# Performance work log

Measured on AMD Instinct MI355X. Metric: run time of the kernel, lower is better.

Reference implementation:

```python
import jax, jax.numpy as jnp
import numpy as np

B, E, T, MAX_LEN = 8192, 1024, 64, 20
EPS = 1e-08


def setup_inputs() -> dict:
    key = jax.random.key(0)
    ks = jax.random.split(key, 8)
    s = 1.0 / np.sqrt(E)
    return {
        "h_t": jax.random.normal(ks[0], (B, E), dtype=jnp.float32),
        "testing": 0,
        "emb": jax.random.normal(ks[1], (T, E), dtype=jnp.float32),
        "W_ih": jax.random.uniform(ks[2], (4 * E, E), minval=-s, maxval=s, dtype=jnp.float32),
        "W_hh": jax.random.uniform(ks[3], (4 * E, E), minval=-s, maxval=s, dtype=jnp.float32),
        "b_ih": jax.random.uniform(ks[4], (4 * E,), minval=-s, maxval=s, dtype=jnp.float32),
        "b_hh": jax.random.uniform(ks[5], (4 * E,), minval=-s, maxval=s, dtype=jnp.float32),
        "W1": jax.random.uniform(ks[6], (T, E), minval=-s, maxval=s, dtype=jnp.float32),
        "b1": jax.random.uniform(ks[7], (T,), minval=-s, maxval=s, dtype=jnp.float32),
    }


def reference(h_t, testing, emb, W_ih, W_hh, b_ih, b_hh, W1, b1):
    batch = h_t.shape[0]
    c0 = jnp.zeros_like(h_t)
    tok0 = jnp.zeros((batch,), dtype=jnp.int32)

    def step(carry, key_i):
        h, c, last = carry
        x = emb[last]  # [B, E] embedding lookup
        gates = x @ W_ih.T + b_ih + h @ W_hh.T + b_hh  # [B, 4E]
        i_g, f_g, g_g, o_g = jnp.split(gates, 4, axis=1)  # PyTorch LSTMCell gate order i,f,g,o
        i_g = jax.nn.sigmoid(i_g)
        f_g = jax.nn.sigmoid(f_g)
        g_g = jnp.tanh(g_g)
        o_g = jax.nn.sigmoid(o_g)
        c = f_g * c + i_g * g_g
        h = o_g * jnp.tanh(c)
        logits = h @ W1.T + b1  # [B, T]
        probs = jax.nn.softmax(logits, axis=1)
        greedy = jnp.argmax(probs, axis=1)
        if testing:
            a = greedy
            log_g = jnp.zeros((batch,), dtype=probs.dtype)
        else:
            a = jax.random.categorical(key_i, logits, axis=1)  # multinomial(probs, 1)
            log_g = jnp.log(jnp.take_along_axis(probs, a[:, None], axis=1))[:, 0]
        matches = (greedy == a).sum()
        p = probs + EPS
        ent = -(p * jnp.log(p)).sum()
        return (h, c, a), (log_g, a, ent, matches)

    keys = jax.random.split(jax.random.key(42), MAX_LEN)
    (_, _, _), (log_gs, toks, ents, matches) = jax.lax.scan(step, (h_t, c0, tok0), keys)
    utterance = toks.T  # [B, MAX_LEN]
    entropy = ents.sum()
    matches_argmax_count = matches.sum()
    stochastic_draws_count = batch * MAX_LEN
    return (log_gs, utterance, entropy, matches_argmax_count, stochastic_draws_count)
```

## Files before the change

### kernel.cpp

```cpp
#include <hip/hip_runtime.h>
#include <hip/hip_bf16.h>
#include <stdint.h>
#include <math.h>

#define BB   8192
#define EE   1024
#define GG   4096
#define TTK  64
#define LLEN 20

#define PRNG_PARTITIONABLE 1

typedef __attribute__((ext_vector_type(8)))  __bf16 bf16x8;
typedef __attribute__((ext_vector_type(4)))  __bf16 bf16x4;
typedef __attribute__((ext_vector_type(16))) float  f32x16;

__host__ __device__ __forceinline__ void tf2x32(unsigned k0, unsigned k1,
                                                unsigned x0, unsigned x1,
                                                unsigned& o0, unsigned& o1) {
  unsigned ks2 = k0 ^ k1 ^ 0x1BD11BDAu;
#define TFR(r) { x0 += x1; x1 = (x1 << (r)) | (x1 >> (32 - (r))); x1 ^= x0; }
  x0 += k0; x1 += k1;
  TFR(13) TFR(15) TFR(26) TFR(6)  x0 += k1;  x1 += ks2 + 1u;
  TFR(17) TFR(29) TFR(16) TFR(24) x0 += ks2; x1 += k0 + 2u;
  TFR(13) TFR(15) TFR(26) TFR(6)  x0 += k0;  x1 += k1 + 3u;
  TFR(17) TFR(29) TFR(16) TFR(24) x0 += k1;  x1 += ks2 + 4u;
  TFR(13) TFR(15) TFR(26) TFR(6)  x0 += ks2; x1 += k0 + 5u;
#undef TFR
  o0 = x0; o1 = x1;
}

__device__ __forceinline__ float wave_max64(float v) {
#pragma unroll
  for (int o = 32; o > 0; o >>= 1) v = fmaxf(v, __shfl_xor(v, o));
  return v;
}
__device__ __forceinline__ float wave_sum64(float v) {
#pragma unroll
  for (int o = 32; o > 0; o >>= 1) v += __shfl_xor(v, o);
  return v;
}
__device__ __forceinline__ void wave_argmax64(float v, int i, float& rv, int& ri) {
  rv = v; ri = i;
#pragma unroll
  for (int o = 32; o > 0; o >>= 1) {
    float ov = __shfl_xor(rv, o);
    int   oi = __shfl_xor(ri, o);
    if (ov > rv || (ov == rv && oi < ri)) { rv = ov; ri = oi; }
  }
}

__global__ void split3_kernel(const float* __restrict__ in, __bf16* __restrict__ s0,
                              __bf16* __restrict__ s1, __bf16* __restrict__ s2, int n) {
  int i = blockIdx.x * blockDim.x + threadIdx.x;
  int stride = gridDim.x * blockDim.x;
  for (; i < n; i += stride) {
    float x = in[i];
    __bf16 a = (__bf16)x; float r1 = x - (float)a;
    __bf16 b = (__bf16)r1; float r2 = r1 - (float)b;
    s0[i] = a; s1[i] = b; s2[i] = (__bf16)r2;
  }
}

__global__ __launch_bounds__(256)
void embw_kernel(const float* __restrict__ emb, const float* __restrict__ Wih,
                 const float* __restrict__ bih, float* __restrict__ embW,
                 float* __restrict__ ent_acc, int* __restrict__ match_acc) {
  if (blockIdx.x == 0 && threadIdx.x == 0) { *ent_acc = 0.0f; *match_acc = 0; }
  __shared__ float hsm[64][36];
  __shared__ float wsm[64][65];
  const int j0 = blockIdx.x * 32;
  const int tid = threadIdx.x;
  const int wv = tid >> 6, lane = tid & 63;
  float acc[8];
#pragma unroll
  for (int r = 0; r < 8; r++) acc[r] = 0.0f;

  for (int k0 = 0; k0 < EE; k0 += 64) {
    {
      int row = tid >> 3, kb = (tid & 7) * 8;
      const float4* p = reinterpret_cast<const float4*>(Wih + (size_t)(j0 + row) * EE + k0 + kb);
      float4 v0 = p[0], v1 = p[1];
      hsm[kb + 0][row] = v0.x; hsm[kb + 1][row] = v0.y; hsm[kb + 2][row] = v0.z; hsm[kb + 3][row] = v0.w;
      hsm[kb + 4][row] = v1.x; hsm[kb + 5][row] = v1.y; hsm[kb + 6][row] = v1.z; hsm[kb + 7][row] = v1.w;
      int tr = tid >> 2, kc = (tid & 3) * 16;
      const float4* q = reinterpret_cast<const float4*>(emb + (size_t)tr * EE + k0 + kc);
#pragma unroll
      for (int i = 0; i < 4; i++) {
        float4 a = q[i];
        wsm[tr][kc + i * 4 + 0] = a.x; wsm[tr][kc + i * 4 + 1] = a.y;
        wsm[tr][kc + i * 4 + 2] = a.z; wsm[tr][kc + i * 4 + 3] = a.w;
      }
    }
    __syncthreads();
#pragma unroll
    for (int k = 0; k < 64; k++) {
      float w0 = wsm[lane][k];
      float4 va = *reinterpret_cast<const float4*>(&hsm[k][wv * 8]);
      float4 vb = *reinterpret_cast<const float4*>(&hsm[k][wv * 8 + 4]);
      acc[0] = fmaf(va.x, w0, acc[0]); acc[1] = fmaf(va.y, w0, acc[1]);
      acc[2] = fmaf(va.z, w0, acc[2]); acc[3] = fmaf(va.w, w0, acc[3]);
      acc[4] = fmaf(vb.x, w0, acc[4]); acc[5] = fmaf(vb.y, w0, acc[5]);
      acc[6] = fmaf(vb.z, w0, acc[6]); acc[7] = fmaf(vb.w, w0, acc[7]);
    }
    __syncthreads();
  }
#pragma unroll
  for (int r = 0; r < 8; r++) {
    int j = j0 + wv * 8 + r;
    embW[(size_t)lane * GG + j] = __fadd_rn(acc[r], bih[j]);
  }
}

#define AST 104
__global__ __launch_bounds__(256, 2)
void lstm_mfma_kernel(const __bf16* __restrict__ hA0, const __bf16* __restrict__ hA1,
                      const __bf16* __restrict__ hA2,
                      __bf16* __restrict__ hN0, __bf16* __restrict__ hN1,
                      __bf16* __restrict__ hN2,
                      float* __restrict__ cbuf,
                      const __bf16* __restrict__ w0s, const __bf16* __restrict__ w1s,
                      const __bf16* __restrict__ w2s,
                      const float* __restrict__ embW, const float* __restrict__ bhh,
                      const int* __restrict__ tok, int step) {
  __shared__ __bf16 lds[(256 + 128) * AST];
  unsigned bid = blockIdx.x;
  unsigned sw = (bid & 7) * 128 + (bid >> 3);
  const int m = sw >> 5, n = sw & 31;
  const int row0 = m * 256, e0 = n * 32;
  const int tid = threadIdx.x;
  const int w = tid >> 6, l = tid & 63;

  f32x16 acc[2][4];
#pragma unroll
  for (int rt = 0; rt < 2; rt++)
#pragma unroll
    for (int ct = 0; ct < 4; ct++)
#pragma unroll
      for (int q = 0; q < 16; q++) acc[rt][ct][q] = 0.0f;

  const int sr = tid >> 2, sq = tid & 3;
  size_t aG[4]; size_t bG[2];
  __bf16* aD[4]; __bf16* bD[2];
#pragma unroll
  for (int rr = 0; rr < 4; rr++) {
    aG[rr] = (size_t)(row0 + sr + rr * 64) * EE + sq * 8;
    aD[rr] = lds + (sr + rr * 64) * AST + sq * 8;
  }
#pragma unroll
  for (int cc = 0; cc < 2; cc++) {
    int c = sr + cc * 64;
    bG[cc] = (size_t)((c >> 5) * 1024 + e0 + (c & 31)) * EE + sq * 8;
    bD[cc] = lds + (256 + sr + cc * 64) * AST + sq * 8;
  }
  const __bf16* aB = lds + (w * 64 + (l & 31)) * AST + (l >> 5) * 8;
  const __bf16* bB = lds + (256 + (l & 31)) * AST + (l >> 5) * 8;

  for (int kt = 0; kt < 32; ++kt) {
    const int k0 = kt * 32;
#pragma unroll
    for (int rr = 0; rr < 4; rr++) {
      bf16x8 v0 = *(const bf16x8*)(hA0 + aG[rr] + k0);
      bf16x8 v1 = *(const bf16x8*)(hA1 + aG[rr] + k0);
      bf16x8 v2 = *(const bf16x8*)(hA2 + aG[rr] + k0);
      *(bf16x8*)(aD[rr])      = v0;
      *(bf16x8*)(aD[rr] + 32) = v1;
      *(bf16x8*)(aD[rr] + 64) = v2;
    }
#pragma unroll
    for (int cc = 0; cc < 2; cc++) {
      bf16x8 v0 = *(const bf16x8*)(w0s + bG[cc] + k0);
      bf16x8 v1 = *(const bf16x8*)(w1s + bG[cc] + k0);
      bf16x8 v2 = *(const bf16x8*)(w2s + bG[cc] + k0);
      *(bf16x8*)(bD[cc])      = v0;
      *(bf16x8*)(bD[cc] + 32) = v1;
      *(bf16x8*)(bD[cc] + 64) = v2;
    }
    __syncthreads();
#pragma unroll
    for (int kh = 0; kh < 2; kh++) {
      bf16x8 a[2][3];
#pragma unroll
      for (int rt = 0; rt < 2; rt++)
#pragma unroll
        for (int s = 0; s < 3; s++)
          a[rt][s] = *(const bf16x8*)(aB + rt * 32 * AST + s * 32 + kh * 16);
#pragma unroll
      for (int ct = 0; ct < 4; ct++) {
        bf16x8 b0 = *(const bf16x8*)(bB + ct * 32 * AST + 0  + kh * 16);
        bf16x8 b1 = *(const bf16x8*)(bB + ct * 32 * AST + 32 + kh * 16);
        bf16x8 b2 = *(const bf16x8*)(bB + ct * 32 * AST + 64 + kh * 16);
#pragma unroll
        for (int rt = 0; rt < 2; rt++) {
          f32x16 t = acc[rt][ct];
          t = __builtin_amdgcn_mfma_f32_32x32x16_bf16(a[rt][2], b0, t, 0, 0, 0);
          t = __builtin_amdgcn_mfma_f32_32x32x16_bf16(a[rt][0], b2, t, 0, 0, 0);
          t = __builtin_amdgcn_mfma_f32_32x32x16_bf16(a[rt][1], b1, t, 0, 0, 0);
          t = __builtin_amdgcn_mfma_f32_32x32x16_bf16(a[rt][1], b0, t, 0, 0, 0);
          t = __builtin_amdgcn_mfma_f32_32x32x16_bf16(a[rt][0], b1, t, 0, 0, 0);
          t = __builtin_amdgcn_mfma_f32_32x32x16_bf16(a[rt][0], b0, t, 0, 0, 0);
          acc[rt][ct] = t;
        }
      }
    }
    __syncthreads();
  }

  float* eC = ((float*)lds) + w * 2112;
  float* eH = eC + 1056;
  const int e_l = l & 31, half = l >> 5;
  float bh4[4];
#pragma unroll
  for (int g = 0; g < 4; g++) bh4[g] = bhh[g * 1024 + e0 + e_l];

#pragma unroll
  for (int rt = 0; rt < 2; rt++) {
    const int rowbase = row0 + w * 64 + rt * 32;
    {
      int r = l >> 3, ch = l & 7;
#pragma unroll
      for (int q = 0; q < 4; q++) {
        float4 cv;
        if (step == 0) cv = make_float4(0.f, 0.f, 0.f, 0.f);
        else cv = *(const float4*)(cbuf + (size_t)(rowbase + r + q * 8) * EE + e0 + ch * 4);
        *(float4*)(eC + (r + q * 8) * 33 + ch * 4) = cv;
      }
    }
    __syncthreads();
#pragma unroll
    for (int i = 0; i < 16; i++) {
      int rl = (i & 3) + 8 * (i >> 2) + 4 * half;
      int b = rowbase + rl;
      int tk = (step == 0) ? 0 : tok[b];
      const float* er = embW + (size_t)tk * GG;
      float g0 = __fadd_rn(__fadd_rn(er[0 * 1024 + e0 + e_l], acc[rt][0][i]), bh4[0]);
      float g1 = __fadd_rn(__fadd_rn(er[1 * 1024 + e0 + e_l], acc[rt][1][i]), bh4[1]);
      float g2 = __fadd_rn(__fadd_rn(er[2 * 1024 + e0 + e_l], acc[rt][2][i]), bh4[2]);
      float g3 = __fadd_rn(__fadd_rn(er[3 * 1024 + e0 + e_l], acc[rt][3][i]), bh4[3]);
      float ig = 1.0f / (1.0f + expf(-g0));
      float fg = 1.0f / (1.0f + expf(-g1));
      float gg = tanhf(g2);
      float og = 1.0f / (1.0f + expf(-g3));
      float co = eC[rl * 33 + e_l];
      float cn = __fadd_rn(__fmul_rn(fg, co), __fmul_rn(ig, gg));
      float hn = __fmul_rn(og, tanhf(cn));
      eC[rl * 33 + e_l] = cn;
      eH[rl * 33 + e_l] = hn;
    }
    __syncthreads();
    {
      int r = l >> 3, ch = l & 7;
#pragma unroll
      for (int q = 0; q < 4; q++) {
        int rr2 = r + q * 8;
        size_t gb = (size_t)(rowbase + rr2) * EE + e0 + ch * 4;
        *(float4*)(cbuf + gb) = *(const float4*)(eC + rr2 * 33 + ch * 4);
        float4 hv = *(const float4*)(eH + rr2 * 33 + ch * 4);
        float hf[4] = {hv.x, hv.y, hv.z, hv.w};
        bf16x4 o0, o1, o2;
#pragma unroll
        for (int j = 0; j < 4; j++) {
          __bf16 a = (__bf16)hf[j]; float r1 = hf[j] - (float)a;
          __bf16 b = (__bf16)r1;    float r2 = r1 - (float)b;
          o0[j] = a; o1[j] = b; o2[j] = (__bf16)r2;
        }
        *(bf16x4*)(hN0 + gb) = o0;
        *(bf16x4*)(hN1 + gb) = o1;
        *(bf16x4*)(hN2 + gb) = o2;
      }
    }
    __syncthreads();
  }
}

__global__ __launch_bounds__(256, 4)
void lstm_step_kernel(const float* __restrict__ hin, float* __restrict__ hout,
                      float* __restrict__ cbuf, const float* __restrict__ Whh,
                      const float* __restrict__ embW, const float* __restrict__ bhh,
                      const int* __restrict__ tok, int step) {
  __shared__ float hs[32][132];
  __shared__ float ws[32][132];
  const int row0 = blockIdx.x * 128;
  const int e0 = blockIdx.y * 32;
  const int tid = threadIdx.x;
  const int tx = tid & 15, ty = tid >> 4;
  float acc[8][4][2];
#pragma unroll
  for (int r = 0; r < 8; r++)
#pragma unroll
    for (int g = 0; g < 4; g++) { acc[r][g][0] = 0.0f; acc[r][g][1] = 0.0f; }

  const int lr = tid >> 3, lk = (tid & 7) * 4;
  for (int k0 = 0; k0 < EE; k0 += 32) {
#pragma unroll
    for (int rr = 0; rr < 4; rr++) {
      int row = lr + rr * 32;
      float4 v = *reinterpret_cast<const float4*>(hin + (size_t)(row0 + row) * EE + k0 + lk);
      hs[lk + 0][row] = v.x; hs[lk + 1][row] = v.y; hs[lk + 2][row] = v.z; hs[lk + 3][row] = v.w;
      int cg = row;
      int j = (cg >> 5) * 1024 + e0 + (cg & 31);
      float4 u = *reinterpret_cast<const float4*>(Whh + (size_t)j * EE + k0 + lk);
      ws[lk + 0][cg] = u.x; ws[lk + 1][cg] = u.y; ws[lk + 2][cg] = u.z; ws[lk + 3][cg] = u.w;
    }
    __syncthreads();
#pragma unroll
    for (int k = 0; k < 32; k++) {
      float4 va = *reinterpret_cast<const float4*>(&hs[k][ty * 8]);
      float4 vb = *reinterpret_cast<const float4*>(&hs[k][ty * 8 + 4]);
      float a0[8] = {va.x, va.y, va.z, va.w, vb.x, vb.y, vb.z, vb.w};
      float wvv[4][2];
#pragma unroll
      for (int g = 0; g < 4; g++) {
        float2 f2 = *reinterpret_cast<const float2*>(&ws[k][g * 32 + tx * 2]);
        wvv[g][0] = f2.x; wvv[g][1] = f2.y;
      }
#pragma unroll
      for (int r = 0; r < 8; r++)
#pragma unroll
        for (int g = 0; g < 4; g++) {
          acc[r][g][0] = fmaf(a0[r], wvv[g][0], acc[r][g][0]);
          acc[r][g][1] = fmaf(a0[r], wvv[g][1], acc[r][g][1]);
        }
    }
    __syncthreads();
  }
#pragma unroll
  for (int r = 0; r < 8; r++) {
    int b = row0 + ty * 8 + r;
    int tk = (step == 0) ? 0 : tok[b];
    const float* er = embW + (size_t)tk * GG;
#pragma unroll
    for (int x = 0; x < 2; x++) {
      int e = e0 + tx * 2 + x;
      float gate[4];
#pragma unroll
      for (int g = 0; g < 4; g++) {
        int j = g * 1024 + e;
        gate[g] = __fadd_rn(__fadd_rn(er[j], acc[r][g][x]), bhh[j]);
      }
      float ig = 1.0f / (1.0f + expf(-gate[0]));
      float fg = 1.0f / (1.0f + expf(-gate[1]));
      float gg = tanhf(gate[2]);
      float og = 1.0f / (1.0f + expf(-gate[3]));
      size_t idx = (size_t)b * EE + e;
      float cn;
      if (step == 0) cn = __fadd_rn(0.0f, __fmul_rn(ig, gg));
      else           cn = __fadd_rn(__fmul_rn(fg, cbuf[idx]), __fmul_rn(ig, gg));
      cbuf[idx] = cn;
      hout[idx] = __fmul_rn(og, tanhf(cn));
    }
  }
}

template <int HS>
__global__ __launch_bounds__(256)
void sample_kernel_t(const float* __restrict__ hf,
                     const __bf16* __restrict__ h0s, const __bf16* __restrict__ h1s,
                     const __bf16* __restrict__ h2s,
                     const float* __restrict__ W1, const float* __restrict__ b1,
                     int* __restrict__ tok, float* __restrict__ out,
                     float* __restrict__ ent_acc, int* __restrict__ match_acc,
                     int step, unsigned key0, unsigned key1) {
  __shared__ float hsm[64][36];
  __shared__ float wsm[64][65];
  __shared__ float entLds[4];
  __shared__ int   mLds[4];
  const int row0 = blockIdx.x * 32;
  const int tid = threadIdx.x;
  const int wv = tid >> 6, lane = tid & 63;
  float acc[8];
#pragma unroll
  for (int r = 0; r < 8; r++) acc[r] = 0.0f;

  for (int k0 = 0; k0 < EE; k0 += 64) {
    {
      int row = tid >> 3, kb = (tid & 7) * 8;
      if (HS) {
        size_t g = (size_t)(row0 + row) * EE + k0 + kb;
        bf16x8 u0 = *(const bf16x8*)(h0s + g);
        bf16x8 u1 = *(const bf16x8*)(h1s + g);
        bf16x8 u2 = *(const bf16x8*)(h2s + g);
#pragma unroll
        for (int j = 0; j < 8; j++)
          hsm[kb + j][row] = __fadd_rn(__fadd_rn((float)u0[j], (float)u1[j]), (float)u2[j]);
      } else {
        const float4* p = reinterpret_cast<const float4*>(hf + (size_t)(row0 + row) * EE + k0 + kb);
        float4 v0 = p[0], v1 = p[1];
        hsm[kb + 0][row] = v0.x; hsm[kb + 1][row] = v0.y; hsm[kb + 2][row] = v0.z; hsm[kb + 3][row] = v0.w;
        hsm[kb + 4][row] = v1.x; hsm[kb + 5][row] = v1.y; hsm[kb + 6][row] = v1.z; hsm[kb + 7][row] = v1.w;
      }
      int tr = tid >> 2, kc = (tid & 3) * 16;
      const float4* q = reinterpret_cast<const float4*>(W1 + (size_t)tr * EE + k0 + kc);
#pragma unroll
      for (int i = 0; i < 4; i++) {
        float4 a = q[i];
        wsm[tr][kc + i * 4 + 0] = a.x; wsm[tr][kc + i * 4 + 1] = a.y;
        wsm[tr][kc + i * 4 + 2] = a.z; wsm[tr][kc + i * 4 + 3] = a.w;
      }
    }
    __syncthreads();
#pragma unroll
    for (int k = 0; k < 64; k++) {
      float w0 = wsm[lane][k];
      float4 va = *reinterpret_cast<const float4*>(&hsm[k][wv * 8]);
      float4 vb = *reinterpret_cast<const float4*>(&hsm[k][wv * 8 + 4]);
      acc[0] = fmaf(va.x, w0, acc[0]); acc[1] = fmaf(va.y, w0, acc[1]);
      acc[2] = fmaf(va.z, w0, acc[2]); acc[3] = fmaf(va.w, w0, acc[3]);
      acc[4] = fmaf(vb.x, w0, acc[4]); acc[5] = fmaf(vb.y, w0, acc[5]);
      acc[6] = fmaf(vb.z, w0, acc[6]); acc[7] = fmaf(vb.w, w0, acc[7]);
    }
    __syncthreads();
  }

  const float b1v = b1[lane];
  float entLane = 0.0f;
  int mcnt = 0;
#pragma unroll 1
  for (int r = 0; r < 8; r++) {
    int b = row0 + wv * 8 + r;
    float lg = __fadd_rn(acc[r], b1v);
    float mx = wave_max64(lg);
    float e = expf(lg - mx);
    float s = wave_sum64(e);
    float p = e / s;
    float gv; int gi; wave_argmax64(p, lane, gv, gi);
    unsigned nidx = (unsigned)(b * 64 + lane);
    unsigned o0, o1, bits;
#if PRNG_PARTITIONABLE
    tf2x32(key0, key1, 0u, nidx, o0, o1);
    bits = o0 ^ o1;
#else
    const unsigned HALF = (BB * TTK) / 2;
    if (nidx < HALF) { tf2x32(key0, key1, nidx, nidx + HALF, o0, o1); bits = o0; }
    else             { tf2x32(key0, key1, nidx - HALF, nidx, o0, o1); bits = o1; }
#endif
    float f = __uint_as_float((bits >> 9) | 0x3f800000u) - 1.0f;
    float u = fmaxf(1.17549435e-38f, f);
    float gum = -logf(-logf(u));
    float z = __fadd_rn(gum, lg);
    float zv; int zi; wave_argmax64(z, lane, zv, zi);
    float pa = __shfl(p, zi);
    if (lane == 0) {
      out[step * BB + b] = logf(pa);
      out[BB * LLEN + b * LLEN + step] = (float)zi;
      tok[b] = zi;
      if (gi == zi) mcnt++;
    }
    float pp = p + 1e-8f;
    entLane += pp * logf(pp);
  }
  float esum = wave_sum64(entLane);
  if (lane == 0) { entLds[wv] = esum; mLds[wv] = mcnt; }
  __syncthreads();
  if (tid == 0) {
    atomicAdd(ent_acc, entLds[0] + entLds[1] + entLds[2] + entLds[3]);
    atomicAdd(match_acc, mLds[0] + mLds[1] + mLds[2] + mLds[3]);
  }
}

__global__ void finalize_kernel(float* __restrict__ out,
                                const float* __restrict__ ent_acc,
                                const int* __restrict__ match_acc) {
  if (threadIdx.x == 0) {
    out[2 * BB * LLEN + 0] = -(*ent_acc);
    out[2 * BB * LLEN + 1] = (float)(*match_acc);
    out[2 * BB * LLEN + 2] = (float)(BB * LLEN);
  }
}

extern "C" void kernel_launch(void* const* d_in, const int* in_sizes, int n_in,
                              void* d_out, int out_size, void* d_ws, size_t ws_size,
                              hipStream_t stream) {
  const float* h_t = (const float*)d_in[0];
  const float* emb = (const float*)d_in[2];
  const float* Wih = (const float*)d_in[3];
  const float* Whh = (const float*)d_in[4];
  const float* bih = (const float*)d_in[5];
  const float* bhh = (const float*)d_in[6];
  const float* W1  = (const float*)d_in[7];
  const float* b1  = (const float*)d_in[8];
  float* out = (float*)d_out;

  unsigned k0s[LLEN], k1s[LLEN];
#if PRNG_PARTITIONABLE
  for (int s = 0; s < LLEN; s++) {
    unsigned a, b2; tf2x32(0u, 42u, 0u, (unsigned)s, a, b2);
    k0s[s] = a; k1s[s] = b2;
  }
#else
  {
    unsigned bitsArr[40];
    for (int j = 0; j < 20; j++) {
      unsigned a, b2; tf2x32(0u, 42u, (unsigned)j, (unsigned)(j + 20), a, b2);
      bitsArr[j] = a; bitsArr[20 + j] = b2;
    }
    for (int s = 0; s < LLEN; s++) { k0s[s] = bitsArr[2 * s]; k1s[s] = bitsArr[2 * s + 1]; }
  }
#endif

  const size_t NE = (size_t)BB * EE;
  const size_t WN = (size_t)GG * EE;
  const size_t NEED = NE * 4 + 6 * NE * 2 + 3 * WN * 2 + (size_t)TTK * GG * 4 + BB * 4 + 64;

  if (ws_size >= NEED) {
    char* p = (char*)d_ws;
    float*  cbuf = (float*)p;            p += NE * 4;
    __bf16* hA0  = (__bf16*)p;           p += NE * 2;
    __bf16* hA1  = (__bf16*)p;           p += NE * 2;
    __bf16* hA2  = (__bf16*)p;           p += NE * 2;
    __bf16* hB0  = (__bf16*)p;           p += NE * 2;
    __bf16* hB1  = (__bf16*)p;           p += NE * 2;
    __bf16* hB2  = (__bf16*)p;           p += NE * 2;
    __bf16* w0   = (__bf16*)p;           p += WN * 2;
    __bf16* w1   = (__bf16*)p;           p += WN * 2;
    __bf16* w2   = (__bf16*)p;           p += WN * 2;
    float*  embW = (float*)p;            p += (size_t)TTK * GG * 4;
    int*    tok  = (int*)p;              p += BB * 4;
    float*  ent_acc = (float*)p;
    int*    match_acc = (int*)(p + 4);

    hipLaunchKernelGGL(split3_kernel, dim3(512), dim3(256), 0, stream,
                       h_t, hA0, hA1, hA2, (int)NE);
    hipLaunchKernelGGL(split3_kernel, dim3(512), dim3(256), 0, stream,
                       Whh, w0, w1, w2, (int)WN);
    hipLaunchKernelGGL(embw_kernel, dim3(128), dim3(256), 0, stream,
                       emb, Wih, bih, embW, ent_acc, match_acc);
    for (int s = 0; s < LLEN; s++) {
      const __bf16 *r0 = (s & 1) ? hB0 : hA0, *r1 = (s & 1) ? hB1 : hA1, *r2 = (s & 1) ? hB2 : hA2;
      __bf16 *n0 = (s & 1) ? hA0 : hB0, *n1 = (s & 1) ? hA1 : hB1, *n2 = (s & 1) ? hA2 : hB2;
      hipLaunchKernelGGL(lstm_mfma_kernel, dim3(1024), dim3(256), 0, stream,
                         r0, r1, r2, n0, n1, n2, cbuf, w0, w1, w2, embW, bhh, tok, s);
      hipLaunchKernelGGL((sample_kernel_t<1>), dim3(256), dim3(256), 0, stream,
                         (const float*)nullptr, n0, n1, n2, W1, b1, tok, out,
                         ent_acc, match_acc, s, k0s[s], k1s[s]);
    }
    hipLaunchKernelGGL(finalize_kernel, dim3(1), dim3(64), 0, stream,
                       out, ent_acc, match_acc);
  } else {
    float* ws = (float*)d_ws;
    float* h0   = ws;
    float* h1   = ws + NE;
    float* cbuf = ws + 2 * NE;
    float* embW = ws + 3 * NE;
    int*   tok  = (int*)(ws + 3 * NE + (size_t)TTK * GG);
    float* ent_acc = (float*)(tok + BB);
    int*   match_acc = (int*)(ent_acc + 1);

    hipLaunchKernelGGL(embw_kernel, dim3(128), dim3(256), 0, stream,
                       emb, Wih, bih, embW, ent_acc, match_acc);
    for (int s = 0; s < LLEN; s++) {
      const float* hin = (s == 0) ? h_t : ((s & 1) ? h0 : h1);
      float* hout = (s & 1) ? h1 : h0;
      hipLaunchKernelGGL(lstm_step_kernel, dim3(64, 32), dim3(256), 0, stream,
                         hin, hout, cbuf, Whh, embW, bhh, tok, s);
      hipLaunchKernelGGL((sample_kernel_t<0>), dim3(256), dim3(256), 0, stream,
                         hout, (const __bf16*)nullptr, (const __bf16*)nullptr,
                         (const __bf16*)nullptr, W1, b1, tok, out,
                         ent_acc, match_acc, s, k0s[s], k1s[s]);
    }
    hipLaunchKernelGGL(finalize_kernel, dim3(1), dim3(64), 0, stream,
                       out, ent_acc, match_acc);
  }
}
```

Measured before the change: 9.196 ms.

## Double-buffer LSTM GEMM tiles with direct global-to-LDS loads

Replaces the register-staged global-to-LDS copies in the LSTM MFMA kernel with global_load_lds DMA into two LDS buffers. The next K-tile is prefetched while MFMAs run on the current one, and one barrier per iteration is removed. The doubled LDS footprint forces occupancy down to one block per CU, so the kernel now depends on the async prefetch to hide latency instead of a second resident block. It also relies on the barrier correctly waiting for the LDS-DMA loads to complete.

Result: slower. 10.51 ms (+14.3%).

```diff
diff --git a/kernel.cpp b/kernel.cpp
--- a/kernel.cpp
+++ b/kernel.cpp
@@ -50,6 +50,12 @@
   }
 }
 
+__device__ __forceinline__ void gl16(const __bf16* g, __bf16* l) {
+  __builtin_amdgcn_global_load_lds(
+      (const __attribute__((address_space(1))) void*)g,
+      (__attribute__((address_space(3))) void*)l, 16, 0, 0);
+}
+
 __global__ void split3_kernel(const float* __restrict__ in, __bf16* __restrict__ s0,
                               __bf16* __restrict__ s1, __bf16* __restrict__ s2, int n) {
   int i = blockIdx.x * blockDim.x + threadIdx.x;
@@ -112,8 +118,9 @@
   }
 }
 
-#define AST 104
-__global__ __launch_bounds__(256, 2)
+#define AST   104
+#define BUFE  39936
+__global__ __launch_bounds__(256, 1)
 void lstm_mfma_kernel(const __bf16* __restrict__ hA0, const __bf16* __restrict__ hA1,
                       const __bf16* __restrict__ hA2,
                       __bf16* __restrict__ hN0, __bf16* __restrict__ hN1,
@@ -123,7 +130,7 @@
                       const __bf16* __restrict__ w2s,
                       const float* __restrict__ embW, const float* __restrict__ bhh,
                       const int* __restrict__ tok, int step) {
-  __shared__ __bf16 lds[(256 + 128) * AST];
+  __shared__ __bf16 lds[2 * BUFE];
   unsigned bid = blockIdx.x;
   unsigned sw = (bid & 7) * 128 + (bid >> 3);
   const int m = sw >> 5, n = sw & 31;
@@ -139,44 +146,62 @@
 #pragma unroll
       for (int q = 0; q < 16; q++) acc[rt][ct][q] = 0.0f;
 
-  const int sr = tid >> 2, sq = tid & 3;
-  size_t aG[4]; size_t bG[2];
-  __bf16* aD[4]; __bf16* bD[2];
-#pragma unroll
-  for (int rr = 0; rr < 4; rr++) {
-    aG[rr] = (size_t)(row0 + sr + rr * 64) * EE + sq * 8;
-    aD[rr] = lds + (sr + rr * 64) * AST + sq * 8;
-  }
-#pragma unroll
-  for (int cc = 0; cc < 2; cc++) {
-    int c = sr + cc * 64;
-    bG[cc] = (size_t)((c >> 5) * 1024 + e0 + (c & 31)) * EE + sq * 8;
-    bD[cc] = lds + (256 + sr + cc * 64) * AST + sq * 8;
-  }
-  const __bf16* aB = lds + (w * 64 + (l & 31)) * AST + (l >> 5) * 8;
-  const __bf16* bB = lds + (256 + (l & 31)) * AST + (l >> 5) * 8;
+  const __bf16* aSrcP[13];
+  const __bf16* bSrcP[7];
+  const int nB = (w < 2) ? 7 : 6;
+#pragma unroll
+  for (int i = 0; i < 13; i++) {
+    int slot = (w * 13 + i) * 64 + l;
+    int row = slot / 13, chk = slot - row * 13;
+    const __bf16* base;
+    size_t off;
+    if (chk < 12) {
+      int s = chk >> 2, q = chk & 3;
+      base = (s == 0) ? hA0 : (s == 1) ? hA1 : hA2;
+      off = (size_t)(row0 + row) * EE + q * 8;
+    } else { base = hA0; off = 0; }
+    aSrcP[i] = base + off;
+  }
+#pragma unroll
+  for (int i = 0; i < 7; i++) {
+    if (i < nB) {
+      int ib = w + i * 4;
+      int slot = ib * 64 + l;
+      int c = slot / 13, chk = slot - c * 13;
+      const __bf16* base;
+      size_t off;
+      if (chk < 12) {
+        int s = chk >> 2, q = chk & 3;
+        int j = (c >> 5) * 1024 + e0 + (c & 31);
+        base = (s == 0) ? w0s : (s == 1) ? w1s : w2s;
+        off = (size_t)j * EE + q * 8;
+      } else { base = w0s; off = 0; }
+      bSrcP[i] = base + off;
+    }
+  }
+  const int aDstOff = w * 13 * 512;
+  const int bDstOff = 26624 + w * 512;
+
+#define STAGE(BUF, KE) do {                                              \
+    _Pragma("unroll")                                                    \
+    for (int i_ = 0; i_ < 13; i_++)                                      \
+      gl16(aSrcP[i_] + (KE), lds + (BUF) + aDstOff + i_ * 512);          \
+    _Pragma("unroll")                                                    \
+    for (int i_ = 0; i_ < 7; i_++)                                       \
+      if (i_ < nB) gl16(bSrcP[i_] + (KE), lds + (BUF) + bDstOff + i_ * 2048); \
+  } while (0)
+
+  const int aRB = (w * 64 + (l & 31)) * AST + (l >> 5) * 8;
+  const int bRB = (256 + (l & 31)) * AST + (l >> 5) * 8;
+
+  STAGE(0, 0);
 
   for (int kt = 0; kt < 32; ++kt) {
-    const int k0 = kt * 32;
-#pragma unroll
-    for (int rr = 0; rr < 4; rr++) {
-      bf16x8 v0 = *(const bf16x8*)(hA0 + aG[rr] + k0);
-      bf16x8 v1 = *(const bf16x8*)(hA1 + aG[rr] + k0);
-      bf16x8 v2 = *(const bf16x8*)(hA2 + aG[rr] + k0);
-      *(bf16x8*)(aD[rr])      = v0;
-      *(bf16x8*)(aD[rr] + 32) = v1;
-      *(bf16x8*)(aD[rr] + 64) = v2;
-    }
-#pragma unroll
-    for (int cc = 0; cc < 2; cc++) {
-      bf16x8 v0 = *(const bf16x8*)(w0s + bG[cc] + k0);
-      bf16x8 v1 = *(const bf16x8*)(w1s + bG[cc] + k0);
-      bf16x8 v2 = *(const bf16x8*)(w2s + bG[cc] + k0);
-      *(bf16x8*)(bD[cc])      = v0;
-      *(bf16x8*)(bD[cc] + 32) = v1;
-      *(bf16x8*)(bD[cc] + 64) = v2;
-    }
-    __syncthreads();
+    __syncthreads();
+    const int cur = (kt & 1) * BUFE;
+    if (kt < 31) STAGE(cur ^ BUFE, (kt + 1) * 32);
+    const __bf16* aB = lds + cur + aRB;
+    const __bf16* bB = lds + cur + bRB;
 #pragma unroll
     for (int kh = 0; kh < 2; kh++) {
       bf16x8 a[2][3];
@@ -203,8 +228,9 @@
         }
       }
     }
-    __syncthreads();
-  }
+  }
+  __syncthreads();
+#undef STAGE
 
   float* eC = ((float*)lds) + w * 2112;
   float* eH = eC + 1056;
```
